# Performance work log

Measured on AMD Instinct MI355X. Metric: run time of the kernel, lower is better.

## Reference

```python
import jax, jax.numpy as jnp
import numpy as np

ZERO_POINT = 128  # asymmetric int8 zero point
LORA_ALPHA = 16.0
LORA_R = 64
LORA_SCALING = LORA_ALPHA / LORA_R


def setup_inputs() -> dict:
    key = jax.random.key(0)
    k_x, k_w, k_s, k_a, k_b, k_bias = jax.random.split(key, 6)
    B, S, D_in, D_out, R = 64, 1, 8192, 8192, LORA_R
    x = jax.random.normal(k_x, (B, S, D_in), dtype=jnp.float32)
    W_q = jax.random.randint(k_w, (D_out, D_in), 0, 256, dtype=jnp.int32)
    scale = jax.random.uniform(k_s, (D_out,), dtype=jnp.float32) * 0.02
    lora_A = jax.random.normal(k_a, (R, D_in), dtype=jnp.float32) * 0.02
    lora_B = jax.random.normal(k_b, (D_out, R), dtype=jnp.float32) * 0.02
    bias = jax.random.normal(k_bias, (D_out,), dtype=jnp.float32)
    return {"x": x, "W_q": W_q, "scale": scale, "lora_A": lora_A,
            "lora_B": lora_B, "bias": bias}


def reference(x, W_q, scale, lora_A, lora_B, bias):
    # Dequantize frozen base weight: per-output-channel asymmetric int8.
    # W_deq[o, i] = (W_q[o, i] - zero_point) * scale[o]
    W_deq = (W_q.astype(jnp.float32) - ZERO_POINT) * scale[:, None]  # [O, I]
    # Base quantized linear: y = x @ W_deq^T + bias
    base = jnp.einsum('bsi,oi->bso', x, W_deq) + bias  # [B, S, O]
    # LoRA low-rank path: (alpha/r) * (x @ A^T) @ B^T  (dropout = 0.0)
    lora_mid = jnp.einsum('bsi,ri->bsr', x, lora_A)        # [B, S, r]
    lora_out = jnp.einsum('bsr,or->bso', lora_mid, lora_B)  # [B, S, O]
    return base + LORA_SCALING * lora_out
```

## Files before the change

kernel.cpp:

```cpp
#include <hip/hip_runtime.h>
#include <stdint.h>

#define B_ 64
#define K_ 8192
#define O_ 8192
#define R_ 64
#define NT 16
#define KSP 2
#define KHALF (K_ / KSP)
#define BK 128
#define NS2 (KHALF / BK)

typedef __attribute__((ext_vector_type(8))) short s16x8;
typedef __attribute__((ext_vector_type(4))) float f32x4;

__device__ __forceinline__ uint32_t rne_pack(float a, float b) {
  uint32_t ua = __float_as_uint(a), ub = __float_as_uint(b);
  ua += 0x7fffu + ((ua >> 16) & 1u);
  ub += 0x7fffu + ((ub >> 16) & 1u);
  return (ua >> 16) | (ub & 0xffff0000u);
}

__device__ __forceinline__ uint32_t wpack(int w0, int w1) {
  float f0 = (float)(w0 - 128);
  float f1 = (float)(w1 - 128);
  return (__float_as_uint(f0) >> 16) | (__float_as_uint(f1) & 0xffff0000u);
}

__device__ __forceinline__ s16x8 afrag(uint4 x) {
  union { uint4 u; s16x8 v; } r; r.u = x; return r.v;
}

__global__ __launch_bounds__(256) void k_prep(
    const float* __restrict__ x, const float* __restrict__ lora_A,
    uint16_t* __restrict__ xbg, float* __restrict__ mid) {
  const int t = threadIdx.x;
  const int blk = blockIdx.x;

  {
    const size_t base = (size_t)blk * 2048 + (size_t)t * 8;
    float4 v0 = *(const float4*)(x + base);
    float4 v1 = *(const float4*)(x + base + 4);
    uint4 p;
    p.x = rne_pack(v0.x, v0.y);
    p.y = rne_pack(v0.z, v0.w);
    p.z = rne_pack(v1.x, v1.y);
    p.w = rne_pack(v1.z, v1.w);
    *(uint4*)(xbg + base) = p;
  }

  if (blk >= 64) return;

  __shared__ float xs[64][133];
  __shared__ float as_[64][133];
  const int kr0 = blk * 128;
  const int row = t >> 2, seg = t & 3;
#pragma unroll
  for (int j = 0; j < 8; ++j) {
    const int c = seg * 32 + j * 4;
    float4 vx = *(const float4*)(x + (size_t)row * K_ + kr0 + c);
    float4 va = *(const float4*)(lora_A + (size_t)row * K_ + kr0 + c);
    xs[row][c] = vx.x; xs[row][c + 1] = vx.y; xs[row][c + 2] = vx.z; xs[row][c + 3] = vx.w;
    as_[row][c] = va.x; as_[row][c + 1] = va.y; as_[row][c + 2] = va.z; as_[row][c + 3] = va.w;
  }
  __syncthreads();

  const int bg = t >> 4, rg = t & 15;
  const int b0 = bg * 4, r0 = rg * 4;
  float acc[4][4];
#pragma unroll
  for (int i = 0; i < 4; ++i)
#pragma unroll
    for (int j = 0; j < 4; ++j) acc[i][j] = 0.f;

  for (int k = 0; k < 128; ++k) {
    float xv[4], av[4];
#pragma unroll
    for (int i = 0; i < 4; ++i) xv[i] = xs[b0 + i][k];
#pragma unroll
    for (int j = 0; j < 4; ++j) av[j] = as_[r0 + j][k];
#pragma unroll
    for (int i = 0; i < 4; ++i)
#pragma unroll
      for (int j = 0; j < 4; ++j) acc[i][j] += xv[i] * av[j];
  }

#pragma unroll
  for (int i = 0; i < 4; ++i)
#pragma unroll
    for (int j = 0; j < 4; ++j)
      atomicAdd(&mid[(b0 + i) * R_ + (r0 + j)], acc[i][j]);
}

__global__ __launch_bounds__(256, 4) void k_main(
    const int* __restrict__ Wq, const uint16_t* __restrict__ xbg,
    float* __restrict__ part) {
  __shared__ uint16_t wbs[2][NT][132];

  const int t = threadIdx.x;
  const int oc = blockIdx.x >> 1;
  const int ks = blockIdx.x & 1;
  const int o0 = oc * NT;
  const int k0 = ks * KHALF;

  const int wave = t >> 6, lane = t & 63, il = lane & 15, g = lane >> 4;
  const int m0 = wave * 16;
  const int wrow = t >> 4, wseg = t & 15;

  const int* wsrc = Wq + (size_t)(o0 + wrow) * K_ + k0 + wseg * 8;
  const uint16_t* xq = xbg + (size_t)(m0 + il) * K_ + k0 + g * 8;

  int4 rwa0, rwb0, rwa1, rwb1, rwa2, rwb2, rwa3, rwb3;
  uint4 ax00, ax01, ax02, ax03, ax10, ax11, ax12, ax13;

#define LOADW(P, S)                                  \
  do {                                               \
    rwa##P = *(const int4*)(wsrc + (S)*BK);          \
    rwb##P = *(const int4*)(wsrc + (S)*BK + 4);      \
  } while (0)
#define LOADX(Q, S)                                  \
  do {                                               \
    ax##Q##0 = *(const uint4*)(xq + (S)*BK);         \
    ax##Q##1 = *(const uint4*)(xq + (S)*BK + 32);    \
    ax##Q##2 = *(const uint4*)(xq + (S)*BK + 64);    \
    ax##Q##3 = *(const uint4*)(xq + (S)*BK + 96);    \
  } while (0)

  f32x4 acc = {0.f, 0.f, 0.f, 0.f};

  LOADW(0, 0); LOADW(1, 1); LOADW(2, 2); LOADW(3, 3);
  LOADX(0, 0); LOADX(1, 1);

#define PHASE(P, Q)                                                            \
  do {                                                                         \
    const int S = s + P;                                                       \
    uint4 wv;                                                                  \
    wv.x = wpack(rwa##P.x, rwa##P.y); wv.y = wpack(rwa##P.z, rwa##P.w);        \
    wv.z = wpack(rwb##P.x, rwb##P.y); wv.w = wpack(rwb##P.z, rwb##P.w);        \
    *(uint4*)&wbs[S & 1][wrow][wseg * 8] = wv;                                 \
    if (S + 4 < NS2) LOADW(P, S + 4);                                          \
    asm volatile("s_waitcnt lgkmcnt(0)" ::: "memory");                         \
    __builtin_amdgcn_s_barrier();                                              \
    __builtin_amdgcn_sched_barrier(0);                                         \
    s16x8 bf0 = *(const s16x8*)&wbs[S & 1][il][0 * 32 + g * 8];                \
    acc = __builtin_amdgcn_mfma_f32_16x16x32_bf16(afrag(ax##Q##0), bf0, acc, 0, 0, 0); \
    s16x8 bf1 = *(const s16x8*)&wbs[S & 1][il][1 * 32 + g * 8];                \
    acc = __builtin_amdgcn_mfma_f32_16x16x32_bf16(afrag(ax##Q##1), bf1, acc, 0, 0, 0); \
    s16x8 bf2 = *(const s16x8*)&wbs[S & 1][il][2 * 32 + g * 8];                \
    acc = __builtin_amdgcn_mfma_f32_16x16x32_bf16(afrag(ax##Q##2), bf2, acc, 0, 0, 0); \
    s16x8 bf3 = *(const s16x8*)&wbs[S & 1][il][3 * 32 + g * 8];                \
    acc = __builtin_amdgcn_mfma_f32_16x16x32_bf16(afrag(ax##Q##3), bf3, acc, 0, 0, 0); \
    if (S + 2 < NS2) LOADX(Q, S + 2);                                          \
  } while (0)

  for (int s = 0; s < NS2; s += 4) {
    PHASE(0, 0);
    PHASE(1, 1);
    PHASE(2, 0);
    PHASE(3, 1);
  }
#undef LOADW
#undef LOADX
#undef PHASE

  float* pp = part + (size_t)ks * (B_ * O_) + o0 + il;
#pragma unroll
  for (int j = 0; j < 4; ++j)
    pp[(size_t)(m0 + g * 4 + j) * O_] = acc[j];
}

__global__ __launch_bounds__(256) void k_fin(
    const float* __restrict__ part, const float* __restrict__ scale,
    const float* __restrict__ lora_B, const float* __restrict__ bias,
    const float* __restrict__ mid, float* __restrict__ out) {
  __shared__ uint16_t midb[64][72];
  __shared__ uint16_t lob[16][72];

  const int t = threadIdx.x;
  const int o0 = blockIdx.x * 16;
  const int wave = t >> 6;
  const int lane = t & 63;
  const int il = lane & 15;
  const int g = lane >> 4;
  const int m0 = wave * 16;

  {
    const int row = t >> 2;
    const int r0 = (t & 3) * 16;
    const float* mp = mid + row * R_ + r0;
    float4 a0 = *(const float4*)(mp);
    float4 a1 = *(const float4*)(mp + 4);
    float4 a2 = *(const float4*)(mp + 8);
    float4 a3 = *(const float4*)(mp + 12);
    uint4 p0, p1;
    p0.x = rne_pack(a0.x, a0.y); p0.y = rne_pack(a0.z, a0.w);
    p0.z = rne_pack(a1.x, a1.y); p0.w = rne_pack(a1.z, a1.w);
    p1.x = rne_pack(a2.x, a2.y); p1.y = rne_pack(a2.z, a2.w);
    p1.z = rne_pack(a3.x, a3.y); p1.w = rne_pack(a3.z, a3.w);
    *(uint4*)&midb[row][r0] = p0;
    *(uint4*)&midb[row][r0 + 8] = p1;
    if (t < 64) {
      const int row2 = t >> 2;
      const float* lp = lora_B + (size_t)(o0 + row2) * R_ + r0;
      float4 c0 = *(const float4*)(lp);
      float4 c1 = *(const float4*)(lp + 4);
      float4 c2 = *(const float4*)(lp + 8);
      float4 c3 = *(const float4*)(lp + 12);
      uint4 q0, q1;
      q0.x = rne_pack(c0.x, c0.y); q0.y = rne_pack(c0.z, c0.w);
      q0.z = rne_pack(c1.x, c1.y); q0.w = rne_pack(c1.z, c1.w);
      q1.x = rne_pack(c2.x, c2.y); q1.y = rne_pack(c2.z, c2.w);
      q1.z = rne_pack(c3.x, c3.y); q1.w = rne_pack(c3.z, c3.w);
      *(uint4*)&lob[row2][r0] = q0;
      *(uint4*)&lob[row2][r0 + 8] = q1;
    }
  }
  __syncthreads();

  f32x4 acc2 = {0.f, 0.f, 0.f, 0.f};
#pragma unroll
  for (int kf = 0; kf < 2; ++kf) {
    s16x8 am = *(const s16x8*)&midb[m0 + il][kf * 32 + g * 8];
    s16x8 bl = *(const s16x8*)&lob[il][kf * 32 + g * 8];
    acc2 = __builtin_amdgcn_mfma_f32_16x16x32_bf16(am, bl, acc2, 0, 0, 0);
  }

  const float sc = scale[o0 + il];
  const float bi = bias[o0 + il];

#pragma unroll
  for (int j = 0; j < 4; ++j) {
    const int b = m0 + g * 4 + j;
    const size_t idx = (size_t)b * O_ + o0 + il;
    float s = part[idx] + part[(size_t)(B_ * O_) + idx];
    out[idx] = sc * s + bi + 0.25f * acc2[j];
  }
}

extern "C" void kernel_launch(void* const* d_in, const int* in_sizes, int n_in,
                              void* d_out, int out_size, void* d_ws, size_t ws_size,
                              hipStream_t stream) {
  const float* x = (const float*)d_in[0];
  const int* Wq = (const int*)d_in[1];
  const float* scale = (const float*)d_in[2];
  const float* lora_A = (const float*)d_in[3];
  const float* lora_B = (const float*)d_in[4];
  const float* bias = (const float*)d_in[5];
  float* out = (float*)d_out;

  uint16_t* xbg = (uint16_t*)d_ws;
  float* mid = (float*)((char*)d_ws + (2u << 20));
  float* part = (float*)((char*)d_ws + (4u << 20));

  hipMemsetAsync(mid, 0, B_ * R_ * sizeof(float), stream);
  k_prep<<<256, 256, 0, stream>>>(x, lora_A, xbg, mid);
  k_main<<<KSP * (O_ / NT), 256, 0, stream>>>(Wq, xbg, part);
  k_fin<<<O_ / 16, 256, 0, stream>>>(part, scale, lora_B, bias, mid, out);
}
```

Baseline: 103.4 us.

## Widen output tile to 128 columns, stage x in LDS, split K eight ways

Restructures the main GEMM so each 512-thread block covers 128 output channels over one eighth of K. Activations are staged through LDS and shared by all waves, where before every 16-column block re-read its bf16 x slice from global. Weight loads are now nontemporal, since the int32 weights are streamed once. In exchange, the partial-sum buffer grows to eight slices, which adds write and read traffic in the finishing kernel and needs more workspace.

```diff
diff --git a/kernel.cpp b/kernel.cpp
--- a/kernel.cpp
+++ b/kernel.cpp
@@ -5,14 +5,15 @@
 #define K_ 8192
 #define O_ 8192
 #define R_ 64
-#define NT 16
-#define KSP 2
-#define KHALF (K_ / KSP)
-#define BK 128
-#define NS2 (KHALF / BK)
+#define NC 128
+#define KS 8
+#define KSL (K_ / KS)
+#define BK 64
+#define NST (KSL / BK)
 
 typedef __attribute__((ext_vector_type(8))) short s16x8;
 typedef __attribute__((ext_vector_type(4))) float f32x4;
+typedef __attribute__((ext_vector_type(4))) int iv4;
 
 __device__ __forceinline__ uint32_t rne_pack(float a, float b) {
   uint32_t ua = __float_as_uint(a), ub = __float_as_uint(b);
@@ -25,10 +26,6 @@
   float f0 = (float)(w0 - 128);
   float f1 = (float)(w1 - 128);
   return (__float_as_uint(f0) >> 16) | (__float_as_uint(f1) & 0xffff0000u);
-}
-
-__device__ __forceinline__ s16x8 afrag(uint4 x) {
-  union { uint4 u; s16x8 v; } r; r.u = x; return r.v;
 }
 
 __global__ __launch_bounds__(256) void k_prep(
@@ -92,81 +89,102 @@
       atomicAdd(&mid[(b0 + i) * R_ + (r0 + j)], acc[i][j]);
 }
 
-__global__ __launch_bounds__(256, 4) void k_main(
+__global__ __launch_bounds__(512, 4) void k_main(
     const int* __restrict__ Wq, const uint16_t* __restrict__ xbg,
     float* __restrict__ part) {
-  __shared__ uint16_t wbs[2][NT][132];
+  __shared__ uint16_t wls[2][NC][74];
+  __shared__ uint16_t xls[2][B_][74];
 
   const int t = threadIdx.x;
-  const int oc = blockIdx.x >> 1;
-  const int ks = blockIdx.x & 1;
-  const int o0 = oc * NT;
-  const int k0 = ks * KHALF;
-
-  const int wave = t >> 6, lane = t & 63, il = lane & 15, g = lane >> 4;
-  const int m0 = wave * 16;
-  const int wrow = t >> 4, wseg = t & 15;
-
-  const int* wsrc = Wq + (size_t)(o0 + wrow) * K_ + k0 + wseg * 8;
-  const uint16_t* xq = xbg + (size_t)(m0 + il) * K_ + k0 + g * 8;
-
-  int4 rwa0, rwb0, rwa1, rwb1, rwa2, rwb2, rwa3, rwb3;
-  uint4 ax00, ax01, ax02, ax03, ax10, ax11, ax12, ax13;
-
-#define LOADW(P, S)                                  \
-  do {                                               \
-    rwa##P = *(const int4*)(wsrc + (S)*BK);          \
-    rwb##P = *(const int4*)(wsrc + (S)*BK + 4);      \
+  const int w = t >> 6, lane = t & 63, il = lane & 15, g = lane >> 4;
+  const int cg = blockIdx.x >> 3;
+  const int ksb = blockIdx.x & 7;
+  const int o0b = cg * NC;
+  const int kb = ksb * KSL;
+
+  const int wr = lane >> 4;
+  const int wc = (lane & 15) * 4;
+  const int* wp0 = Wq + (size_t)(o0b + w * 16 + 0 + wr) * K_ + kb + wc;
+  const int* wp1 = Wq + (size_t)(o0b + w * 16 + 4 + wr) * K_ + kb + wc;
+  const int* wp2 = Wq + (size_t)(o0b + w * 16 + 8 + wr) * K_ + kb + wc;
+  const int* wp3 = Wq + (size_t)(o0b + w * 16 + 12 + wr) * K_ + kb + wc;
+
+  const int xrow = t >> 3, xco = (t & 7) * 8;
+  const uint16_t* xp = xbg + (size_t)xrow * K_ + kb + xco;
+
+  const int mrow = (w >> 1) * 16 + il;
+  const int nb = (w & 1) * 64;
+
+  iv4 wA0, wA1, wA2, wA3, wB0, wB1, wB2, wB3;
+  uint4 xA, xB;
+
+#define LOADW(P, S)                                                          \
+  do {                                                                       \
+    w##P##0 = __builtin_nontemporal_load((const iv4*)(wp0 + (S) * BK));      \
+    w##P##1 = __builtin_nontemporal_load((const iv4*)(wp1 + (S) * BK));      \
+    w##P##2 = __builtin_nontemporal_load((const iv4*)(wp2 + (S) * BK));      \
+    w##P##3 = __builtin_nontemporal_load((const iv4*)(wp3 + (S) * BK));      \
   } while (0)
-#define LOADX(Q, S)                                  \
-  do {                                               \
-    ax##Q##0 = *(const uint4*)(xq + (S)*BK);         \
-    ax##Q##1 = *(const uint4*)(xq + (S)*BK + 32);    \
-    ax##Q##2 = *(const uint4*)(xq + (S)*BK + 64);    \
-    ax##Q##3 = *(const uint4*)(xq + (S)*BK + 96);    \
+#define LOADX(P, S) x##P = *(const uint4*)(xp + (S) * BK)
+
+  LOADW(A, 0); LOADX(A, 0);
+  LOADW(B, 1); LOADX(B, 1);
+
+  f32x4 ac0 = {0.f,0.f,0.f,0.f}, ac1 = {0.f,0.f,0.f,0.f};
+  f32x4 ac2 = {0.f,0.f,0.f,0.f}, ac3 = {0.f,0.f,0.f,0.f};
+
+#define STEP(P, BUF, S)                                                        \
+  do {                                                                         \
+    uint2 u;                                                                   \
+    u.x = wpack(w##P##0[0], w##P##0[1]); u.y = wpack(w##P##0[2], w##P##0[3]);  \
+    *(uint2*)&wls[BUF][w * 16 + 0 + wr][wc] = u;                               \
+    u.x = wpack(w##P##1[0], w##P##1[1]); u.y = wpack(w##P##1[2], w##P##1[3]);  \
+    *(uint2*)&wls[BUF][w * 16 + 4 + wr][wc] = u;                               \
+    u.x = wpack(w##P##2[0], w##P##2[1]); u.y = wpack(w##P##2[2], w##P##2[3]);  \
+    *(uint2*)&wls[BUF][w * 16 + 8 + wr][wc] = u;                               \
+    u.x = wpack(w##P##3[0], w##P##3[1]); u.y = wpack(w##P##3[2], w##P##3[3]);  \
+    *(uint2*)&wls[BUF][w * 16 + 12 + wr][wc] = u;                              \
+    *(uint4*)&xls[BUF][xrow][xco] = x##P;                                      \
+    __syncthreads();                                                           \
+    if ((S) + 2 < NST) { LOADW(P, (S) + 2); LOADX(P, (S) + 2); }               \
+    s16x8 af0 = *(const s16x8*)&xls[BUF][mrow][0 * 32 + g * 8];                \
+    s16x8 bf0 = *(const s16x8*)&wls[BUF][nb + 0 * 16 + il][0 * 32 + g * 8];    \
+    ac0 = __builtin_amdgcn_mfma_f32_16x16x32_bf16(af0, bf0, ac0, 0, 0, 0);     \
+    s16x8 bf1 = *(const s16x8*)&wls[BUF][nb + 1 * 16 + il][0 * 32 + g * 8];    \
+    ac1 = __builtin_amdgcn_mfma_f32_16x16x32_bf16(af0, bf1, ac1, 0, 0, 0);     \
+    s16x8 bf2 = *(const s16x8*)&wls[BUF][nb + 2 * 16 + il][0 * 32 + g * 8];    \
+    ac2 = __builtin_amdgcn_mfma_f32_16x16x32_bf16(af0, bf2, ac2, 0, 0, 0);     \
+    s16x8 bf3 = *(const s16x8*)&wls[BUF][nb + 3 * 16 + il][0 * 32 + g * 8];    \
+    ac3 = __builtin_amdgcn_mfma_f32_16x16x32_bf16(af0, bf3, ac3, 0, 0, 0);     \
+    s16x8 af1 = *(const s16x8*)&xls[BUF][mrow][1 * 32 + g * 8];                \
+    s16x8 bg0 = *(const s16x8*)&wls[BUF][nb + 0 * 16 + il][1 * 32 + g * 8];    \
+    ac0 = __builtin_amdgcn_mfma_f32_16x16x32_bf16(af1, bg0, ac0, 0, 0, 0);     \
+    s16x8 bg1 = *(const s16x8*)&wls[BUF][nb + 1 * 16 + il][1 * 32 + g * 8];    \
+    ac1 = __builtin_amdgcn_mfma_f32_16x16x32_bf16(af1, bg1, ac1, 0, 0, 0);     \
+    s16x8 bg2 = *(const s16x8*)&wls[BUF][nb + 2 * 16 + il][1 * 32 + g * 8];    \
+    ac2 = __builtin_amdgcn_mfma_f32_16x16x32_bf16(af1, bg2, ac2, 0, 0, 0);     \
+    s16x8 bg3 = *(const s16x8*)&wls[BUF][nb + 3 * 16 + il][1 * 32 + g * 8];    \
+    ac3 = __builtin_amdgcn_mfma_f32_16x16x32_bf16(af1, bg3, ac3, 0, 0, 0);     \
   } while (0)
 
-  f32x4 acc = {0.f, 0.f, 0.f, 0.f};
-
-  LOADW(0, 0); LOADW(1, 1); LOADW(2, 2); LOADW(3, 3);
-  LOADX(0, 0); LOADX(1, 1);
-
-#define PHASE(P, Q)                                                            \
-  do {                                                                         \
-    const int S = s + P;                                                       \
-    uint4 wv;                                                                  \
-    wv.x = wpack(rwa##P.x, rwa##P.y); wv.y = wpack(rwa##P.z, rwa##P.w);        \
-    wv.z = wpack(rwb##P.x, rwb##P.y); wv.w = wpack(rwb##P.z, rwb##P.w);        \
-    *(uint4*)&wbs[S & 1][wrow][wseg * 8] = wv;                                 \
-    if (S + 4 < NS2) LOADW(P, S + 4);                                          \
-    asm volatile("s_waitcnt lgkmcnt(0)" ::: "memory");                         \
-    __builtin_amdgcn_s_barrier();                                              \
-    __builtin_amdgcn_sched_barrier(0);                                         \
-    s16x8 bf0 = *(const s16x8*)&wbs[S & 1][il][0 * 32 + g * 8];                \
-    acc = __builtin_amdgcn_mfma_f32_16x16x32_bf16(afrag(ax##Q##0), bf0, acc, 0, 0, 0); \
-    s16x8 bf1 = *(const s16x8*)&wbs[S & 1][il][1 * 32 + g * 8];                \
-    acc = __builtin_amdgcn_mfma_f32_16x16x32_bf16(afrag(ax##Q##1), bf1, acc, 0, 0, 0); \
-    s16x8 bf2 = *(const s16x8*)&wbs[S & 1][il][2 * 32 + g * 8];                \
-    acc = __builtin_amdgcn_mfma_f32_16x16x32_bf16(afrag(ax##Q##2), bf2, acc, 0, 0, 0); \
-    s16x8 bf3 = *(const s16x8*)&wbs[S & 1][il][3 * 32 + g * 8];                \
-    acc = __builtin_amdgcn_mfma_f32_16x16x32_bf16(afrag(ax##Q##3), bf3, acc, 0, 0, 0); \
-    if (S + 2 < NS2) LOADX(Q, S + 2);                                          \
-  } while (0)
-
-  for (int s = 0; s < NS2; s += 4) {
-    PHASE(0, 0);
-    PHASE(1, 1);
-    PHASE(2, 0);
-    PHASE(3, 1);
+  for (int s = 0; s < NST; s += 2) {
+    STEP(A, 0, s);
+    STEP(B, 1, s + 1);
   }
 #undef LOADW
 #undef LOADX
-#undef PHASE
-
-  float* pp = part + (size_t)ks * (B_ * O_) + o0 + il;
-#pragma unroll
-  for (int j = 0; j < 4; ++j)
-    pp[(size_t)(m0 + g * 4 + j) * O_] = acc[j];
+#undef STEP
+
+  float* pp = part + (size_t)ksb * (B_ * O_);
+#pragma unroll
+  for (int jj = 0; jj < 4; ++jj) {
+    const int b = (w >> 1) * 16 + g * 4 + jj;
+    float* row = pp + (size_t)b * O_ + o0b + nb + il;
+    row[0]  = ac0[jj];
+    row[16] = ac1[jj];
+    row[32] = ac2[jj];
+    row[48] = ac3[jj];
+  }
 }
 
 __global__ __launch_bounds__(256) void k_fin(
@@ -232,7 +250,9 @@
   for (int j = 0; j < 4; ++j) {
     const int b = m0 + g * 4 + j;
     const size_t idx = (size_t)b * O_ + o0 + il;
-    float s = part[idx] + part[(size_t)(B_ * O_) + idx];
+    float s = 0.f;
+#pragma unroll
+    for (int k = 0; k < KS; ++k) s += part[(size_t)k * (B_ * O_) + idx];
     out[idx] = sc * s + bi + 0.25f * acc2[j];
   }
 }
@@ -254,6 +274,6 @@
 
   hipMemsetAsync(mid, 0, B_ * R_ * sizeof(float), stream);
   k_prep<<<256, 256, 0, stream>>>(x, lora_A, xbg, mid);
-  k_main<<<KSP * (O_ / NT), 256, 0, stream>>>(Wq, xbg, part);
+  k_main<<<KS * (O_ / NC), 512, 0, stream>>>(Wq, xbg, part);
   k_fin<<<O_ / 16, 256, 0, stream>>>(part, scale, lora_B, bias, mid, out);
 }
```

Result: faster. 97.09 us (-6.1%).
